# Performance work log

Measured on AMD Instinct MI355X. Metric: run time of the kernel, lower is better.

## Reference

```python
import jax, jax.numpy as jnp
import numpy as np

N_HEADS = 16
N_KV_HEADS = 8
N_REP = 2
HEAD_DIM = 128
SOFTCAP = 50.0
NEG_INF = -2.3819763e38
ROPE_BASE = 10000.0


def _rotate_half(x):
    x1, x2 = jnp.split(x, 2, axis=-1)
    return jnp.concatenate((-x2, x1), axis=-1)


def _rope_cos_sin(seq_len, dtype):
    # Gemma2RotaryEmbedding: inv_freq over even dims, emb = cat(freqs, freqs)
    inv_freq = 1.0 / (ROPE_BASE ** (jnp.arange(0, HEAD_DIM, 2, dtype=jnp.float32) / HEAD_DIM))
    freqs = jnp.arange(seq_len, dtype=jnp.float32)[:, None] * inv_freq[None, :]  # [s, hd/2]
    emb = jnp.concatenate((freqs, freqs), axis=-1)  # [s, hd]
    return jnp.cos(emb).astype(dtype), jnp.sin(emb).astype(dtype)


def setup_inputs() -> dict:
    key = jax.random.key(0)
    ks = jax.random.split(key, 5)
    b, s, d = 2, 2048, 2048
    w_scale = 0.02
    return {
        "x": jax.random.normal(ks[0], (b, s, d), dtype=jnp.float32),
        "wq": jax.random.normal(ks[1], (N_HEADS * HEAD_DIM, d), dtype=jnp.float32) * w_scale,
        "wk": jax.random.normal(ks[2], (N_KV_HEADS * HEAD_DIM, d), dtype=jnp.float32) * w_scale,
        "wv": jax.random.normal(ks[3], (N_KV_HEADS * HEAD_DIM, d), dtype=jnp.float32) * w_scale,
        "wo": jax.random.normal(ks[4], (d, N_HEADS * HEAD_DIM), dtype=jnp.float32) * w_scale,
    }


def reference(x, wq, wk, wv, wo):
    b, s, d = x.shape
    # QKV projections (linear_fn = plain x @ W.T)
    xq = (x @ wq.T).reshape(b, s, N_HEADS, HEAD_DIM).transpose(0, 2, 1, 3)      # [b,h,s,hd]
    xk = (x @ wk.T).reshape(b, s, N_KV_HEADS, HEAD_DIM).transpose(0, 2, 1, 3)   # [b,kv,s,hd]
    xv = (x @ wv.T).reshape(b, s, N_KV_HEADS, HEAD_DIM).transpose(0, 2, 1, 3)
    # Gemma2 rotary on q, k
    cos, sin = _rope_cos_sin(s, x.dtype)  # [s,hd] each, broadcast over b,h
    xq = xq * cos + _rotate_half(xq) * sin
    xk = xk * cos + _rotate_half(xk) * sin
    # repeat_kv: expand kv heads to n_heads
    keys = jnp.repeat(xk, N_REP, axis=1)
    values = jnp.repeat(xv, N_REP, axis=1)
    # scores with scaling and Gemma2 logit softcapping
    scale = float(HEAD_DIM) ** -0.5
    scores = jnp.einsum("bhsd,bhtd->bhst", xq * scale, keys)
    scores = jnp.tanh(scores / SOFTCAP) * SOFTCAP
    # causal additive mask [s, t]
    q_pos = jnp.arange(s)[:, None]
    k_pos = jnp.arange(s)[None, :]
    mask = jnp.where(k_pos <= q_pos, 0.0, NEG_INF).astype(jnp.float32)
    scores = scores + mask  # broadcast over [b,h]
    probs = jax.nn.softmax(scores.astype(jnp.float32), axis=-1).astype(xq.dtype)
    out = jnp.einsum("bhst,bhtd->bhsd", probs, values)
    out = out.transpose(0, 2, 1, 3).reshape(b, s, N_HEADS * HEAD_DIM)
    return out @ wo.T
```

## Files before the change

### kernel.cpp

```cpp
#include <hip/hip_runtime.h>
#include <stdint.h>
#include <stddef.h>

#define S_LEN   2048
#define DMODEL  2048
#define NHEADS  16
#define NKVH    8
#define HD      128
#define QPRE 1.7677669529663688e-3f
#define C1 72.13475204444817f

typedef __attribute__((ext_vector_type(8))) short  short8;
typedef __attribute__((ext_vector_type(4))) float  float4v;

static __device__ __forceinline__ unsigned short f2bf(float f) {
  union { float f; unsigned int u; } v; v.f = f;
  unsigned int u = v.u;
  u += 0x7fffu + ((u >> 16) & 1u);
  return (unsigned short)(u >> 16);
}
static __device__ __forceinline__ float bf2f(unsigned short b) {
  union { unsigned int u; float f; } v; v.u = ((unsigned int)b) << 16;
  return v.f;
}
static __device__ __forceinline__ void gload_lds16(const void* g, void* l) {
  __builtin_amdgcn_global_load_lds(
      (const __attribute__((address_space(1))) void*)g,
      (__attribute__((address_space(3))) void*)l, 16, 0, 0);
}

__global__ __launch_bounds__(256) void cvt_all(
    const float* __restrict__ x,  const float* __restrict__ wq,
    const float* __restrict__ wk, const float* __restrict__ wv,
    const float* __restrict__ wo,
    ushort4* __restrict__ xb, ushort4* __restrict__ wcat,
    ushort4* __restrict__ wob) {
  int i = blockIdx.x * 256 + threadIdx.x;
  const float4* src; ushort4* dst; int j;
  if (i < 2097152)      { src = (const float4*)x;  dst = xb;             j = i; }
  else if (i < 3145728) { src = (const float4*)wq; dst = wcat;           j = i - 2097152; }
  else if (i < 3670016) { src = (const float4*)wk; dst = wcat + 1048576; j = i - 3145728; }
  else if (i < 4194304) { src = (const float4*)wv; dst = wcat + 1572864; j = i - 3670016; }
  else                  { src = (const float4*)wo; dst = wob;            j = i - 4194304; }
  float4 v = src[j];
  ushort4 o;
  o.x = f2bf(v.x); o.y = f2bf(v.y); o.z = f2bf(v.z); o.w = f2bf(v.w);
  dst[j] = o;
}

__global__ __launch_bounds__(256, 2) void gemm_bf16(
    const unsigned short* __restrict__ A,
    const unsigned short* __restrict__ B,
    void* __restrict__ Cout, int N, int mode) {
  const int t    = threadIdx.x;
  const int lane = t & 63;
  const int w    = t >> 6;
  const int l15  = lane & 15;
  const int quad = lane >> 4;
  const int m0   = blockIdx.y * 128;
  const int n0   = blockIdx.x * 128;
  const int wm   = (w >> 1) * 64;
  const int wn   = (w & 1) * 64;

  __shared__ unsigned short At[128 * 32];
  __shared__ unsigned short Bt[128 * 32];

  float4v acc[4][4];
#pragma unroll
  for (int mt = 0; mt < 4; ++mt)
#pragma unroll
    for (int nt = 0; nt < 4; ++nt)
      acc[mt][nt] = (float4v){0.f, 0.f, 0.f, 0.f};

  const unsigned short* Abase = A + (size_t)m0 * DMODEL;
  const unsigned short* Bbase = B + (size_t)n0 * DMODEL;
  const int srow = w * 16 + (lane >> 2);
  const int sch  = (lane & 3) * 8;

  for (int k0 = 0; k0 < DMODEL; k0 += 32) {
#pragma unroll
    for (int r = 0; r < 2; ++r) {
      gload_lds16(Abase + (size_t)(r * 64 + srow) * DMODEL + k0 + sch,
                  At + (r * 256 + w * 64) * 8);
      gload_lds16(Bbase + (size_t)(r * 64 + srow) * DMODEL + k0 + sch,
                  Bt + (r * 256 + w * 64) * 8);
    }
    __syncthreads();
    short8 af[4], bf[4];
#pragma unroll
    for (int mt = 0; mt < 4; ++mt)
      af[mt] = *(const short8*)(At + (wm + mt * 16 + l15) * 32 + quad * 8);
#pragma unroll
    for (int nt = 0; nt < 4; ++nt)
      bf[nt] = *(const short8*)(Bt + (wn + nt * 16 + l15) * 32 + quad * 8);
#pragma unroll
    for (int mt = 0; mt < 4; ++mt)
#pragma unroll
      for (int nt = 0; nt < 4; ++nt)
        acc[mt][nt] = __builtin_amdgcn_mfma_f32_16x16x32_bf16(
            af[mt], bf[nt], acc[mt][nt], 0, 0, 0);
    __syncthreads();
  }

  if (mode == 2) {
    float* C = (float*)Cout;
#pragma unroll
    for (int mt = 0; mt < 4; ++mt) {
      int row = m0 + wm + mt * 16 + quad * 4;
#pragma unroll
      for (int nt = 0; nt < 4; ++nt) {
        int col = n0 + wn + nt * 16 + l15;
#pragma unroll
        for (int r2 = 0; r2 < 4; ++r2)
          C[(size_t)(row + r2) * N + col] = acc[mt][nt][r2];
      }
    }
  } else {
    unsigned short* C = (unsigned short*)Cout;
#pragma unroll
    for (int mt = 0; mt < 4; ++mt) {
      int row0 = m0 + wm + mt * 16 + quad * 4;
      int b = row0 >> 11, s0 = row0 & (S_LEN - 1);
#pragma unroll
      for (int nt = 0; nt < 4; ++nt) {
        int col = n0 + wn + nt * 16 + l15;
        if (col < 2048) {
          int head = col >> 7, d = col & (HD - 1);
#pragma unroll
          for (int r2 = 0; r2 < 4; ++r2)
            C[((size_t)(b * 16 + head) * S_LEN + s0 + r2) * HD + d] =
                f2bf(acc[mt][nt][r2]);
        } else if (col < 3072) {
          int c2 = col - 2048;
          int kvh = c2 >> 7, d = c2 & (HD - 1);
#pragma unroll
          for (int r2 = 0; r2 < 4; ++r2)
            C[8388608 + ((size_t)(b * 8 + kvh) * S_LEN + s0 + r2) * HD + d] =
                f2bf(acc[mt][nt][r2]);
        } else {
          int c2 = col - 3072;
          int kvh = c2 >> 7, d = c2 & (HD - 1);
          ushort4 pk;
          pk.x = f2bf(acc[mt][nt][0]); pk.y = f2bf(acc[mt][nt][1]);
          pk.z = f2bf(acc[mt][nt][2]); pk.w = f2bf(acc[mt][nt][3]);
          *(ushort4*)&C[12582912 + ((size_t)(b * 8 + kvh) * HD + d) * S_LEN + s0] = pk;
        }
      }
    }
  }
}

__global__ __launch_bounds__(256) void rope_kernel(unsigned short* __restrict__ Q,
                                                   unsigned short* __restrict__ Kc) {
  int gt = blockIdx.x * 256 + threadIdx.x;
  int r = gt >> 6;
  int j = gt & 63;
  const int QROWS = 2 * NHEADS * S_LEN;
  bool isQ = (r < QROWS);
  unsigned short* p = isQ ? (Q + (size_t)r * HD)
                          : (Kc + (size_t)(r - QROWS) * HD);
  int pos = r & (S_LEN - 1);
  float inv = exp2f(-(float)j * 0.20762050593046868f);
  float ang = (float)pos * inv;
  float c = cosf(ang), s = sinf(ang);
  float sc = isQ ? QPRE : 1.0f;
  float x1 = bf2f(p[j]), x2 = bf2f(p[j + 64]);
  p[j]      = f2bf((x1 * c - x2 * s) * sc);
  p[j + 64] = f2bf((x2 * c + x1 * s) * sc);
}

__global__ __launch_bounds__(256, 2) void attn_kernel(
    const unsigned short* __restrict__ Q,
    const unsigned short* __restrict__ Kc,
    const unsigned short* __restrict__ Vt,
    unsigned short* __restrict__ Aout) {
  const int t    = threadIdx.x;
  const int lane = t & 63;
  const int w    = t >> 6;
  const int l15  = lane & 15;
  const int quad = lane >> 4;
  const int bh = blockIdx.x;
  const int pp = blockIdx.y;
  const int b = bh >> 4, h = bh & 15, kv = h >> 1;
  const int qtA = pp, qtB = 31 - pp;
  const int q0A = qtA * 64, q0B = qtB * 64;
  const int ntB = qtB + 1;

  __shared__ unsigned short Kt[2][64 * 128];
  __shared__ unsigned short Vts[2][128 * 64];
  __shared__ unsigned short Pt[4 * 2 * 1024];

  int offK[4], offV[4];
#pragma unroll
  for (int i = 0; i < 4; ++i) {
    int g = i * 256 + t;
    int rK = g >> 4, cK = (g & 15) ^ (rK & 7);
    offK[i] = rK * HD + cK * 8;
    int rV = g >> 3, cV = (g & 7) ^ (rV & 7);
    offV[i] = rV * S_LEN + cV * 8;
  }

  const unsigned short* QA = Q + ((size_t)(b * NHEADS + h) * S_LEN + q0A + w * 16) * HD;
  const unsigned short* QB = Q + ((size_t)(b * NHEADS + h) * S_LEN + q0B + w * 16) * HD;
  short8 qfA[4], qfB[4];
#pragma unroll
  for (int kk = 0; kk < 4; ++kk) {
    qfA[kk] = *(const short8*)&QA[l15 * HD + kk * 32 + quad * 8];
    qfB[kk] = *(const short8*)&QB[l15 * HD + kk * 32 + quad * 8];
  }

  float4v oA[8], oB[8];
#pragma unroll
  for (int nth = 0; nth < 8; ++nth) {
    oA[nth] = (float4v){0.f, 0.f, 0.f, 0.f};
    oB[nth] = (float4v){0.f, 0.f, 0.f, 0.f};
  }
  float lsA = 0.f, lsB = 0.f;

  const unsigned short* kg0 = Kc + (size_t)(b * NKVH + kv) * S_LEN * HD;
  const unsigned short* vg0 = Vt + (size_t)(b * NKVH + kv) * HD * S_LEN;
  unsigned short* PB = Pt + (w * 2 + 0) * 1024;
  unsigned short* PA = Pt + (w * 2 + 1) * 1024;

  auto stage = [&](int kt, int buf) {
    const unsigned short* kgp = kg0 + (size_t)kt * 64 * HD;
    const unsigned short* vgp = vg0 + (size_t)kt * 64;
#pragma unroll
    for (int i = 0; i < 4; ++i)
      gload_lds16(kgp + offK[i], &Kt[buf][(i * 256 + w * 64) * 8]);
#pragma unroll
    for (int i = 0; i < 4; ++i)
      gload_lds16(vgp + offV[i], &Vts[buf][(i * 256 + w * 64) * 8]);
  };

  auto softcap = [&](float x) -> float {
    float xx = __builtin_amdgcn_fmed3f(x, -0.26f, 0.26f);
    float x2 = xx * xx;
    float u = __builtin_fmaf(0.13333334f, x2, -0.33333334f);
    float v = __builtin_fmaf(u, x2, 1.0f);
    return __builtin_amdgcn_exp2f((C1 * xx) * v);
  };

  stage(0, 0);
  for (int kt = 0; kt < ntB; ++kt) {
    const int cur = kt & 1;
    __syncthreads();
    if (kt + 1 < ntB) stage(kt + 1, cur ^ 1);
    const bool doA   = (kt <= qtA);
    const bool diagA = (kt == qtA);
    const bool diagB = (kt == qtB);
    const unsigned short* Kb = Kt[cur];
    const unsigned short* Vb = Vts[cur];

#pragma unroll
    for (int ntk = 0; ntk < 4; ++ntk) {
      int pb = l15 * 64 + (((ntk * 2 + (quad >> 1)) ^ (l15 & 7)) * 8) + (quad & 1) * 4;
      short8 kf[4];
#pragma unroll
      for (int kk = 0; kk < 4; ++kk)
        kf[kk] = *(const short8*)
            &Kb[(ntk * 16 + l15) * HD + (((kk * 4 + quad) ^ (l15 & 7)) * 8)];

      if (diagB && (ntk * 16 > w * 16 + 15)) {
        uint2 z; z.x = 0u; z.y = 0u;
        *(uint2*)&PB[pb] = z;
      } else {
        float4v s0 = (float4v){0.f, 0.f, 0.f, 0.f};
#pragma unroll
        for (int kk = 0; kk < 4; ++kk)
          s0 = __builtin_amdgcn_mfma_f32_16x16x32_bf16(kf[kk], qfB[kk], s0, 0, 0, 0);
        float pv[4];
#pragma unroll
        for (int r = 0; r < 4; ++r) {
          float p = softcap(s0[r]);
          if (diagB)
            p = (ntk * 16 + quad * 4 + r <= w * 16 + l15) ? p : 0.f;
          lsB += p;
          pv[r] = p;
        }
        union { float f; unsigned u; } u0, u1, u2, u3;
        u0.f = pv[0]; u1.f = pv[1]; u2.f = pv[2]; u3.f = pv[3];
        uint2 pk;
        pk.x = __builtin_amdgcn_perm(u1.u, u0.u, 0x07060302);
        pk.y = __builtin_amdgcn_perm(u3.u, u2.u, 0x07060302);
        *(uint2*)&PB[pb] = pk;
      }

      if (doA) {
        if (diagA && (ntk * 16 > w * 16 + 15)) {
          uint2 z; z.x = 0u; z.y = 0u;
          *(uint2*)&PA[pb] = z;
        } else {
          float4v s0 = (float4v){0.f, 0.f, 0.f, 0.f};
#pragma unroll
          for (int kk = 0; kk < 4; ++kk)
            s0 = __builtin_amdgcn_mfma_f32_16x16x32_bf16(kf[kk], qfA[kk], s0, 0, 0, 0);
          float pv[4];
#pragma unroll
          for (int r = 0; r < 4; ++r) {
            float p = softcap(s0[r]);
            if (diagA)
              p = (ntk * 16 + quad * 4 + r <= w * 16 + l15) ? p : 0.f;
            lsA += p;
            pv[r] = p;
          }
          union { float f; unsigned u; } u0, u1, u2, u3;
          u0.f = pv[0]; u1.f = pv[1]; u2.f = pv[2]; u3.f = pv[3];
          uint2 pk;
          pk.x = __builtin_amdgcn_perm(u1.u, u0.u, 0x07060302);
          pk.y = __builtin_amdgcn_perm(u3.u, u2.u, 0x07060302);
          *(uint2*)&PA[pb] = pk;
        }
      }
    }

#pragma unroll
    for (int kk = 0; kk < 2; ++kk) {
      int sw = ((kk * 4 + quad) ^ (l15 & 7)) * 8;
      short8 pB0 = *(const short8*)&PB[l15 * 64 + sw];
      short8 pA0;
      if (doA) pA0 = *(const short8*)&PA[l15 * 64 + sw];
#pragma unroll
      for (int nth = 0; nth < 8; ++nth) {
        short8 vf = *(const short8*)&Vb[(nth * 16 + l15) * 64 + sw];
        oB[nth] = __builtin_amdgcn_mfma_f32_16x16x32_bf16(pB0, vf, oB[nth], 0, 0, 0);
        if (doA)
          oA[nth] = __builtin_amdgcn_mfma_f32_16x16x32_bf16(pA0, vf, oA[nth], 0, 0, 0);
      }
    }
  }

#pragma unroll
  for (int tile = 0; tile < 2; ++tile) {
    float ls = tile ? lsA : lsB;
    float4v* oo = tile ? oA : oB;
    int q0 = tile ? q0A : q0B;
    float v = ls;
    v += __shfl_xor(v, 16, 64);
    v += __shfl_xor(v, 32, 64);
    float inv = __builtin_amdgcn_rcpf(v);
    float iv[4];
#pragma unroll
    for (int r = 0; r < 4; ++r) iv[r] = __shfl(inv, quad * 4 + r, 64);
    unsigned short* ob = Aout + (size_t)(b * S_LEN + q0 + w * 16) * DMODEL + h * HD;
#pragma unroll
    for (int nth = 0; nth < 8; ++nth) {
#pragma unroll
      for (int r = 0; r < 4; ++r) {
        int row = quad * 4 + r;
        ob[(size_t)row * DMODEL + nth * 16 + l15] = f2bf(oo[nth][r] * iv[r]);
      }
    }
  }
}

extern "C" void kernel_launch(void* const* d_in, const int* in_sizes, int n_in,
                              void* d_out, int out_size, void* d_ws, size_t ws_size,
                              hipStream_t stream) {
  const float* x  = (const float*)d_in[0];
  const float* wq = (const float*)d_in[1];
  const float* wk = (const float*)d_in[2];
  const float* wv = (const float*)d_in[3];
  const float* wo = (const float*)d_in[4];

  char* ws = (char*)d_ws;
  unsigned short* xb   = (unsigned short*)(ws + 0);
  unsigned short* wcat = (unsigned short*)(ws + 16777216);
  unsigned short* wob  = (unsigned short*)(ws + 33554432);
  unsigned short* QKV  = (unsigned short*)(ws + 41943040);
  unsigned short* AO   = (unsigned short*)(ws + 75497472);

  unsigned short* Qw = QKV;
  unsigned short* Kw = QKV + 8388608;
  unsigned short* Vw = QKV + 12582912;

  cvt_all<<<20480, 256, 0, stream>>>(x, wq, wk, wv, wo,
                                     (ushort4*)xb, (ushort4*)wcat, (ushort4*)wob);

  gemm_bf16<<<dim3(32, 32), 256, 0, stream>>>(xb, wcat, QKV, 4096, 3);

  rope_kernel<<<24576, 256, 0, stream>>>(Qw, Kw);

  attn_kernel<<<dim3(32, 16), 256, 0, stream>>>(Qw, Kw, Vw, AO);

  gemm_bf16<<<dim3(16, 32), 256, 0, stream>>>(AO, wob, d_out, 2048, 2);
}
```

Before: 338.1 us.

## Add 256x256-tile pipelined QKV GEMM with direct-to-LDS loads and swizzle

Replaces the 128-tile QKV projection GEMM with a dedicated 256x256 tile, 512-thread kernel. It double-buffers K tiles using global-to-LDS loads with an XOR-swizzled layout and interleaves MFMA quadrants with staged loads and s_setprio. Block IDs are remapped for locality. This targets higher data reuse and better overlap of memory and compute in the largest GEMM, in exchange for higher register and LDS pressure and more complex barrier sequencing.

```diff
diff --git a/kernel.cpp b/kernel.cpp
--- a/kernel.cpp
+++ b/kernel.cpp
@@ -102,52 +102,206 @@
     __syncthreads();
   }
 
-  if (mode == 2) {
-    float* C = (float*)Cout;
+  float* C = (float*)Cout;
+#pragma unroll
+  for (int mt = 0; mt < 4; ++mt) {
+    int row = m0 + wm + mt * 16 + quad * 4;
+#pragma unroll
+    for (int nt = 0; nt < 4; ++nt) {
+      int col = n0 + wn + nt * 16 + l15;
+#pragma unroll
+      for (int r2 = 0; r2 < 4; ++r2)
+        C[(size_t)(row + r2) * N + col] = acc[mt][nt][r2];
+    }
+  }
+}
+
+__global__ __launch_bounds__(512, 2) void gemm256_qkv(
+    const unsigned short* __restrict__ A,
+    const unsigned short* __restrict__ B,
+    unsigned short* __restrict__ C) {
+  const int t    = threadIdx.x;
+  const int lane = t & 63;
+  const int w    = t >> 6;
+  const int l15  = lane & 15;
+  const int quad = lane >> 4;
+
+  const int id  = blockIdx.x;
+  const int swz = (id & 7) * 32 + (id >> 3);
+  const int m0  = (swz >> 4) * 256;
+  const int n0  = (swz & 15) * 256;
+
+  __shared__ unsigned short sm[2][2][2][128 * 64];
+
+  const int wm  = w >> 2;
+  const int wnq = w & 3;
+  const int hB  = wnq >> 1;
+  const int wnl = (wnq & 1) * 64;
+
+  int soff[2];
+#pragma unroll
+  for (int i = 0; i < 2; ++i) {
+    int P = (w * 2 + i) * 64 + lane;
+    int r = P >> 3;
+    int lc = (P & 7) ^ (r & 7);
+    soff[i] = r * DMODEL + lc * 8;
+  }
+  const unsigned short* Ab = A + (size_t)m0 * DMODEL;
+  const unsigned short* Bb = B + (size_t)n0 * DMODEL;
+
+  auto stage = [&](int mat, int half, int buf, int kt) {
+    const unsigned short* g =
+        (mat ? Bb : Ab) + (size_t)half * 128 * DMODEL + kt * 64;
+    unsigned short* l = &sm[buf][mat][half][(w * 2) * 512];
+#pragma unroll
+    for (int i = 0; i < 2; ++i)
+      gload_lds16(g + soff[i], l + i * 512);
+  };
+
+  float4v acc[2][2][4][2];
+#pragma unroll
+  for (int qm = 0; qm < 2; ++qm)
+#pragma unroll
+    for (int qn = 0; qn < 2; ++qn)
+#pragma unroll
+      for (int mt = 0; mt < 4; ++mt)
+#pragma unroll
+        for (int nt = 0; nt < 2; ++nt)
+          acc[qm][qn][mt][nt] = (float4v){0.f, 0.f, 0.f, 0.f};
+
+  stage(0, 0, 0, 0); stage(0, 1, 0, 0); stage(1, 0, 0, 0); stage(1, 1, 0, 0);
+  stage(0, 0, 1, 1); stage(0, 1, 1, 1); stage(1, 0, 1, 1);
+  asm volatile("s_waitcnt vmcnt(6)" ::: "memory");
+  __builtin_amdgcn_s_barrier();
+
+  const int NT = DMODEL / 64;
+#pragma unroll 1
+  for (int j = 0; j < NT; ++j) {
+    const int c = j & 1;
+    const unsigned short* As = &sm[c][0][wm][0];
+    const unsigned short* Bs = &sm[c][1][hB][0];
+    short8 af[4][2], bf0[2][2], bf1[2][2];
+
+#pragma unroll
+    for (int mt = 0; mt < 4; ++mt)
+#pragma unroll
+      for (int kk = 0; kk < 2; ++kk) {
+        int r = mt * 16 + l15;
+        af[mt][kk] = *(const short8*)&As[r * 64 + (((kk * 4 + quad) ^ (r & 7)) * 8)];
+      }
+#pragma unroll
+    for (int nt = 0; nt < 2; ++nt)
+#pragma unroll
+      for (int kk = 0; kk < 2; ++kk) {
+        int r = wnl + nt * 16 + l15;
+        bf0[nt][kk] = *(const short8*)&Bs[r * 64 + (((kk * 4 + quad) ^ (r & 7)) * 8)];
+      }
+    if (j + 1 < NT) stage(1, 1, c ^ 1, j + 1);
+    __builtin_amdgcn_s_barrier();
+    __builtin_amdgcn_s_setprio(1);
+#pragma unroll
+    for (int mt = 0; mt < 4; ++mt)
+#pragma unroll
+      for (int nt = 0; nt < 2; ++nt)
+#pragma unroll
+        for (int kk = 0; kk < 2; ++kk)
+          acc[0][0][mt][nt] = __builtin_amdgcn_mfma_f32_16x16x32_bf16(
+              af[mt][kk], bf0[nt][kk], acc[0][0][mt][nt], 0, 0, 0);
+    __builtin_amdgcn_s_setprio(0);
+    __builtin_amdgcn_s_barrier();
+
+#pragma unroll
+    for (int nt = 0; nt < 2; ++nt)
+#pragma unroll
+      for (int kk = 0; kk < 2; ++kk) {
+        int r = wnl + 32 + nt * 16 + l15;
+        bf1[nt][kk] = *(const short8*)&Bs[r * 64 + (((kk * 4 + quad) ^ (r & 7)) * 8)];
+      }
+    __builtin_amdgcn_s_barrier();
+    __builtin_amdgcn_s_setprio(1);
+#pragma unroll
+    for (int mt = 0; mt < 4; ++mt)
+#pragma unroll
+      for (int nt = 0; nt < 2; ++nt)
+#pragma unroll
+        for (int kk = 0; kk < 2; ++kk)
+          acc[0][1][mt][nt] = __builtin_amdgcn_mfma_f32_16x16x32_bf16(
+              af[mt][kk], bf1[nt][kk], acc[0][1][mt][nt], 0, 0, 0);
+    __builtin_amdgcn_s_setprio(0);
+    __builtin_amdgcn_s_barrier();
+
+#pragma unroll
+    for (int mt = 0; mt < 4; ++mt)
+#pragma unroll
+      for (int kk = 0; kk < 2; ++kk) {
+        int r = 64 + mt * 16 + l15;
+        af[mt][kk] = *(const short8*)&As[r * 64 + (((kk * 4 + quad) ^ (r & 7)) * 8)];
+      }
+    __builtin_amdgcn_s_barrier();
+    __builtin_amdgcn_s_setprio(1);
+#pragma unroll
+    for (int mt = 0; mt < 4; ++mt)
+#pragma unroll
+      for (int nt = 0; nt < 2; ++nt)
+#pragma unroll
+        for (int kk = 0; kk < 2; ++kk)
+          acc[1][0][mt][nt] = __builtin_amdgcn_mfma_f32_16x16x32_bf16(
+              af[mt][kk], bf0[nt][kk], acc[1][0][mt][nt], 0, 0, 0);
+    __builtin_amdgcn_s_setprio(0);
+    __builtin_amdgcn_s_barrier();
+
+    if (j + 2 < NT) {
+      stage(0, 0, c, j + 2); stage(0, 1, c, j + 2); stage(1, 0, c, j + 2);
+    }
+    __builtin_amdgcn_s_barrier();
+    __builtin_amdgcn_s_setprio(1);
+#pragma unroll
+    for (int mt = 0; mt < 4; ++mt)
+#pragma unroll
+      for (int nt = 0; nt < 2; ++nt)
+#pragma unroll
+        for (int kk = 0; kk < 2; ++kk)
+          acc[1][1][mt][nt] = __builtin_amdgcn_mfma_f32_16x16x32_bf16(
+              af[mt][kk], bf1[nt][kk], acc[1][1][mt][nt], 0, 0, 0);
+    __builtin_amdgcn_s_setprio(0);
+    if (j + 2 < NT)      { asm volatile("s_waitcnt vmcnt(6)" ::: "memory"); }
+    else if (j + 1 < NT) { asm volatile("s_waitcnt vmcnt(0)" ::: "memory"); }
+    __builtin_amdgcn_s_barrier();
+  }
+
+#pragma unroll
+  for (int qm = 0; qm < 2; ++qm)
 #pragma unroll
     for (int mt = 0; mt < 4; ++mt) {
-      int row = m0 + wm + mt * 16 + quad * 4;
-#pragma unroll
-      for (int nt = 0; nt < 4; ++nt) {
-        int col = n0 + wn + nt * 16 + l15;
-#pragma unroll
-        for (int r2 = 0; r2 < 4; ++r2)
-          C[(size_t)(row + r2) * N + col] = acc[mt][nt][r2];
-      }
-    }
-  } else {
-    unsigned short* C = (unsigned short*)Cout;
-#pragma unroll
-    for (int mt = 0; mt < 4; ++mt) {
-      int row0 = m0 + wm + mt * 16 + quad * 4;
+      int row0 = m0 + wm * 128 + qm * 64 + mt * 16 + quad * 4;
       int b = row0 >> 11, s0 = row0 & (S_LEN - 1);
 #pragma unroll
-      for (int nt = 0; nt < 4; ++nt) {
-        int col = n0 + wn + nt * 16 + l15;
-        if (col < 2048) {
-          int head = col >> 7, d = col & (HD - 1);
-#pragma unroll
-          for (int r2 = 0; r2 < 4; ++r2)
-            C[((size_t)(b * 16 + head) * S_LEN + s0 + r2) * HD + d] =
-                f2bf(acc[mt][nt][r2]);
-        } else if (col < 3072) {
-          int c2 = col - 2048;
-          int kvh = c2 >> 7, d = c2 & (HD - 1);
-#pragma unroll
-          for (int r2 = 0; r2 < 4; ++r2)
-            C[8388608 + ((size_t)(b * 8 + kvh) * S_LEN + s0 + r2) * HD + d] =
-                f2bf(acc[mt][nt][r2]);
-        } else {
-          int c2 = col - 3072;
-          int kvh = c2 >> 7, d = c2 & (HD - 1);
-          ushort4 pk;
-          pk.x = f2bf(acc[mt][nt][0]); pk.y = f2bf(acc[mt][nt][1]);
-          pk.z = f2bf(acc[mt][nt][2]); pk.w = f2bf(acc[mt][nt][3]);
-          *(ushort4*)&C[12582912 + ((size_t)(b * 8 + kvh) * HD + d) * S_LEN + s0] = pk;
+      for (int qn = 0; qn < 2; ++qn)
+#pragma unroll
+        for (int nt = 0; nt < 2; ++nt) {
+          int col = n0 + wnq * 64 + qn * 32 + nt * 16 + l15;
+          float4v v = acc[qm][qn][mt][nt];
+          if (col < 2048) {
+            int head = col >> 7, d = col & (HD - 1);
+#pragma unroll
+            for (int r2 = 0; r2 < 4; ++r2)
+              C[((size_t)(b * 16 + head) * S_LEN + s0 + r2) * HD + d] = f2bf(v[r2]);
+          } else if (col < 3072) {
+            int c2 = col - 2048;
+            int kvh = c2 >> 7, d = c2 & (HD - 1);
+#pragma unroll
+            for (int r2 = 0; r2 < 4; ++r2)
+              C[8388608 + ((size_t)(b * 8 + kvh) * S_LEN + s0 + r2) * HD + d] = f2bf(v[r2]);
+          } else {
+            int c2 = col - 3072;
+            int kvh = c2 >> 7, d = c2 & (HD - 1);
+            ushort4 pk;
+            pk.x = f2bf(v[0]); pk.y = f2bf(v[1]);
+            pk.z = f2bf(v[2]); pk.w = f2bf(v[3]);
+            *(ushort4*)&C[12582912 + ((size_t)(b * 8 + kvh) * HD + d) * S_LEN + s0] = pk;
+          }
         }
-      }
-    }
-  }
+    }
 }
 
 __global__ __launch_bounds__(256) void rope_kernel(unsigned short* __restrict__ Q,
@@ -377,7 +531,7 @@
   cvt_all<<<20480, 256, 0, stream>>>(x, wq, wk, wv, wo,
                                      (ushort4*)xb, (ushort4*)wcat, (ushort4*)wob);
 
-  gemm_bf16<<<dim3(32, 32), 256, 0, stream>>>(xb, wcat, QKV, 4096, 3);
+  gemm256_qkv<<<256, 512, 0, stream>>>(xb, wcat, QKV);
 
   rope_kernel<<<24576, 256, 0, stream>>>(Qw, Kw);
 
```

After: 323.3 us. 1.05x faster.
